# Kernel tuning notes

Measured on AMD Instinct MI355X. Metric: run time of the kernel, lower is better.

## Reference

```python
import jax, jax.numpy as jnp
import numpy as np
import math

S, B, D, H = 1024, 4, 1024, 16
DH = D // H


def setup_inputs() -> dict:
    key = jax.random.key(0)
    ks = jax.random.split(key, 8)
    hidden_states = jax.random.normal(ks[0], (S, B, D), dtype=jnp.float32)
    u = jax.random.uniform(ks[1], (B, 1, 1, S), dtype=jnp.float32)
    attention_mask = jnp.where(u < 0.2, jnp.float32(-10000.0), jnp.float32(0.0))
    std = 0.02
    Wq = jax.random.normal(ks[2], (D, D), dtype=jnp.float32) * std
    bq = jnp.zeros((D,), dtype=jnp.float32)
    Wk = jax.random.normal(ks[3], (D, D), dtype=jnp.float32) * std
    bk = jnp.zeros((D,), dtype=jnp.float32)
    Wv = jax.random.normal(ks[4], (D, D), dtype=jnp.float32) * std
    bv = jnp.zeros((D,), dtype=jnp.float32)
    return {"hidden_states": hidden_states, "attention_mask": attention_mask,
            "Wq": Wq, "bq": bq, "Wk": Wk, "bk": bk, "Wv": Wv, "bv": bv}


def _split_heads(x):
    # [S,B,D] -> [B,H,S,DH]
    s, b, d = x.shape
    return x.reshape(s, b, H, DH).transpose(1, 2, 0, 3)


def reference(hidden_states, attention_mask, Wq, bq, Wk, bk, Wv, bv):
    scale = 1.0 / math.sqrt(DH)
    q = _split_heads(hidden_states @ Wq.T + bq)  # [B,H,S,DH]
    k = _split_heads(hidden_states @ Wk.T + bk)
    v = _split_heads(hidden_states @ Wv.T + bv)
    # scaled scores + additive mask (mask [B,1,1,S] broadcasts over heads, query pos)
    scores = jnp.einsum('bhsd,bhtd->bhst', q, k) * scale + attention_mask  # [B,H,S,S]
    probs = jax.nn.softmax(scores, axis=-1)
    # NOTE: original forward's dropout block is a no-op (only reshapes), so none applied
    ctx = jnp.einsum('bhst,bhtd->bhsd', probs, v)  # [B,H,S,DH]
    # -> [S,B,D]
    return ctx.transpose(2, 0, 1, 3).reshape(S, B, D)
```

## Files before the change

### kernel.cpp

```cpp
#include <hip/hip_runtime.h>
#include <hip/hip_bf16.h>

#define S_LEN  1024
#define BATCH  4
#define DMODEL 1024
#define NHEAD  16
#define DHEAD  64
#define NROWS  (S_LEN*BATCH)

typedef __bf16 bf16;
typedef __bf16 bf16x4 __attribute__((ext_vector_type(4)));
typedef __bf16 bf16x8 __attribute__((ext_vector_type(8)));
typedef float  f32x4  __attribute__((ext_vector_type(4)));

#define AS1 __attribute__((address_space(1)))
#define AS3 __attribute__((address_space(3)))

__device__ __forceinline__ void gload16(const bf16* g, bf16* l) {
  __builtin_amdgcn_global_load_lds((const AS1 void*)g, (AS3 void*)l, 16, 0, 0);
}

__global__ __launch_bounds__(256) void cvt_all(
    const float* __restrict__ hs, const float* __restrict__ wq,
    const float* __restrict__ wk, const float* __restrict__ wv,
    bf16* __restrict__ Xb, bf16* __restrict__ Wb)
{
  const int b = blockIdx.x;
  const float* src; bf16* dst; int i;
  if (b < 2048)      { src = hs; dst = Xb;                           i = b*256        + threadIdx.x; }
  else if (b < 2560) { src = wq; dst = Wb;                           i = (b-2048)*256 + threadIdx.x; }
  else if (b < 3072) { src = wk; dst = Wb + (size_t)DMODEL*DMODEL;   i = (b-2560)*256 + threadIdx.x; }
  else               { src = wv; dst = Wb + (size_t)2*DMODEL*DMODEL; i = (b-3072)*256 + threadIdx.x; }
  const float4* s4 = (const float4*)src;
  float4 a = s4[2*i], c = s4[2*i+1];
  bf16x8 o;
  o[0]=(bf16)a.x; o[1]=(bf16)a.y; o[2]=(bf16)a.z; o[3]=(bf16)a.w;
  o[4]=(bf16)c.x; o[5]=(bf16)c.y; o[6]=(bf16)c.z; o[7]=(bf16)c.w;
  ((bf16x8*)dst)[i] = o;
}

#define BM 128
#define BN 128
#define BK 32

__global__ __launch_bounds__(256) void qkv_gemm(
    const bf16* __restrict__ X, const bf16* __restrict__ Wcat,
    const float* __restrict__ bq, const float* __restrict__ bk, const float* __restrict__ bv,
    bf16* __restrict__ Qo, bf16* __restrict__ Ko, bf16* __restrict__ Vo)
{
  __shared__ __align__(16) bf16 As[BM*BK];
  __shared__ __align__(16) bf16 Bs[BN*BK];

  const int tid  = threadIdx.x;
  const int row0 = blockIdx.x * BM;
  const int col0 = blockIdx.y * BN;
  const int wsel = col0 >> 10;
  const int coln = col0 & 1023;

  const int wv   = tid >> 6;
  const int lane = tid & 63;
  const int lg   = lane >> 4;
  const int lr   = lane & 15;
  const int wr   = (wv >> 1) << 6;
  const int wc   = (wv & 1) << 6;

  const int c0 = tid, c1 = tid + 256;
  const size_t gA0 = (size_t)(row0 + (c0>>2))*DMODEL + (size_t)((c0&3)<<3);
  const size_t gA1 = (size_t)(row0 + (c1>>2))*DMODEL + (size_t)((c1&3)<<3);
  const size_t gB0 = (size_t)(col0 + (c0>>2))*DMODEL + (size_t)((c0&3)<<3);
  const size_t gB1 = (size_t)(col0 + (c1>>2))*DMODEL + (size_t)((c1&3)<<3);
  const int wb = (tid >> 6) << 6;
  bf16* lA0 = As + (size_t)wb*8;
  bf16* lA1 = As + (size_t)(wb+256)*8;
  bf16* lB0 = Bs + (size_t)wb*8;
  bf16* lB1 = Bs + (size_t)(wb+256)*8;

  f32x4 acc[4][4];
  #pragma unroll
  for (int mi=0; mi<4; ++mi)
    #pragma unroll
    for (int ni=0; ni<4; ++ni)
      acc[mi][ni] = (f32x4){0.f,0.f,0.f,0.f};

  for (int k0 = 0; k0 < DMODEL; k0 += BK) {
    __syncthreads();
    gload16(X    + gA0 + k0, lA0);
    gload16(X    + gA1 + k0, lA1);
    gload16(Wcat + gB0 + k0, lB0);
    gload16(Wcat + gB1 + k0, lB1);
    __syncthreads();

    bf16x8 af[4], bfr[4];
    #pragma unroll
    for (int mi=0; mi<4; ++mi)
      af[mi] = *(const bf16x8*)&As[(wr + mi*16 + lr)*BK + lg*8];
    #pragma unroll
    for (int ni=0; ni<4; ++ni)
      bfr[ni] = *(const bf16x8*)&Bs[(wc + ni*16 + lr)*BK + lg*8];

    #pragma unroll
    for (int mi=0; mi<4; ++mi)
      #pragma unroll
      for (int ni=0; ni<4; ++ni)
        acc[mi][ni] = __builtin_amdgcn_mfma_f32_16x16x32_bf16(af[mi], bfr[ni], acc[mi][ni], 0, 0, 0);
  }

  const float* bias = (wsel==0) ? bq : ((wsel==1) ? bk : bv);
  bf16* Out = (wsel==0) ? Qo : ((wsel==1) ? Ko : Vo);

  #pragma unroll
  for (int ni=0; ni<4; ++ni) {
    const int co = coln + wc + ni*16 + lr;
    const float bias_v = bias[co];
    const int h  = co >> 6;
    const int dh = co & 63;
    #pragma unroll
    for (int mi=0; mi<4; ++mi) {
      #pragma unroll
      for (int p=0; p<4; ++p) {
        const int gr = row0 + wr + mi*16 + lg*4 + p;
        const int s_ = gr >> 2;
        const int b_ = gr & 3;
        Out[((size_t)(b_*NHEAD + h)*S_LEN + s_)*DHEAD + dh] = (bf16)(acc[mi][ni][p] + bias_v);
      }
    }
  }
}

#define LPAD 72

__global__ __launch_bounds__(256) void attn_mfma(
    const bf16* __restrict__ Q, const bf16* __restrict__ K, const bf16* __restrict__ V,
    const float* __restrict__ mask, float* __restrict__ out)
{
  __shared__ __align__(16) bf16 Qs[64][LPAD];
  __shared__ __align__(16) bf16 Ks[64][LPAD];
  __shared__ __align__(16) bf16 Vt[64][LPAD];
  __shared__ __align__(16) bf16 Pw[4][16][LPAD];
  __shared__ float Ms[64];

  const int bh   = blockIdx.x;
  const int b_   = bh >> 4;
  const int h    = bh & 15;
  const int tid  = threadIdx.x;
  const int wv   = tid >> 6;
  const int lane = tid & 63;
  const int lg   = lane >> 4;
  const int lr   = lane & 15;
  const int q0   = blockIdx.y * 64;

  const bf16* Qb = Q + ((size_t)bh*S_LEN + q0)*DHEAD;
  const bf16* Kb = K + (size_t)bh*S_LEN*DHEAD;
  const bf16* Vb = V + (size_t)bh*S_LEN*DHEAD;
  const float* mb = mask + (size_t)b_*S_LEN;

  {
    const int r = tid >> 2, c = (tid & 3) << 4;
    const bf16x8* src = (const bf16x8*)&Qb[(size_t)r*DHEAD + c];
    *(bf16x8*)&Qs[r][c]   = src[0];
    *(bf16x8*)&Qs[r][c+8] = src[1];
  }
  __syncthreads();
  bf16x8 qa0 = *(const bf16x8*)&Qs[wv*16 + lr][lg*8];
  bf16x8 qa1 = *(const bf16x8*)&Qs[wv*16 + lr][32 + lg*8];

  f32x4 ctx[4];
  #pragma unroll
  for (int nt=0; nt<4; ++nt) ctx[nt] = (f32x4){0.f,0.f,0.f,0.f};
  float lsum[4] = {0.f,0.f,0.f,0.f};

  const int vr = tid & 63, vc = (tid >> 6) << 4;

  for (int t0 = 0; t0 < S_LEN; t0 += 64) {
    __syncthreads();
    {
      const int r = tid >> 2, c = (tid & 3) << 4;
      const bf16x8* src = (const bf16x8*)&Kb[(size_t)(t0+r)*DHEAD + c];
      *(bf16x8*)&Ks[r][c]   = src[0];
      *(bf16x8*)&Ks[r][c+8] = src[1];
    }
    {
      const bf16x8* src = (const bf16x8*)&Vb[(size_t)(t0+vr)*DHEAD + vc];
      bf16x8 v0 = src[0], v1 = src[1];
      #pragma unroll
      for (int i=0;i<8;++i){ Vt[vc+i][vr] = v0[i]; Vt[vc+8+i][vr] = v1[i]; }
    }
    if (tid < 64) Ms[tid] = mb[t0 + tid];
    __syncthreads();

    f32x4 sacc[4];
    #pragma unroll
    for (int nt=0; nt<4; ++nt) {
      sacc[nt] = (f32x4){0.f,0.f,0.f,0.f};
      bf16x8 kb0 = *(const bf16x8*)&Ks[nt*16 + lr][lg*8];
      bf16x8 kb1 = *(const bf16x8*)&Ks[nt*16 + lr][32 + lg*8];
      sacc[nt] = __builtin_amdgcn_mfma_f32_16x16x32_bf16(qa0, kb0, sacc[nt], 0,0,0);
      sacc[nt] = __builtin_amdgcn_mfma_f32_16x16x32_bf16(qa1, kb1, sacc[nt], 0,0,0);
    }

    #pragma unroll
    for (int nt=0; nt<4; ++nt) {
      const float mval = Ms[nt*16 + lr];
      #pragma unroll
      for (int p=0; p<4; ++p) {
        const float pr = __expf(fmaf(sacc[nt][p], 0.125f, mval));
        lsum[p] += pr;
        Pw[wv][lg*4 + p][nt*16 + lr] = (bf16)pr;
      }
    }

    {
      bf16x8 pa0 = *(const bf16x8*)&Pw[wv][lr][lg*8];
      bf16x8 pa1 = *(const bf16x8*)&Pw[wv][lr][32 + lg*8];
      #pragma unroll
      for (int nt=0; nt<4; ++nt) {
        bf16x8 vb0 = *(const bf16x8*)&Vt[nt*16 + lr][lg*8];
        bf16x8 vb1 = *(const bf16x8*)&Vt[nt*16 + lr][32 + lg*8];
        ctx[nt] = __builtin_amdgcn_mfma_f32_16x16x32_bf16(pa0, vb0, ctx[nt], 0,0,0);
        ctx[nt] = __builtin_amdgcn_mfma_f32_16x16x32_bf16(pa1, vb1, ctx[nt], 0,0,0);
      }
    }
  }

  #pragma unroll
  for (int p=0; p<4; ++p) {
    float s = lsum[p];
    s += __shfl_xor(s, 1); s += __shfl_xor(s, 2);
    s += __shfl_xor(s, 4); s += __shfl_xor(s, 8);
    lsum[p] = s;
  }

  #pragma unroll
  for (int p=0; p<4; ++p) {
    const float inv = 1.f / lsum[p];
    const int qg = q0 + wv*16 + lg*4 + p;
    float* op = out + ((size_t)qg*BATCH + b_)*DMODEL + h*DHEAD;
    #pragma unroll
    for (int nt=0; nt<4; ++nt) op[nt*16 + lr] = ctx[nt][p] * inv;
  }
}

extern "C" void kernel_launch(void* const* d_in, const int* in_sizes, int n_in,
                              void* d_out, int out_size, void* d_ws, size_t ws_size,
                              hipStream_t stream) {
  const float* hs   = (const float*)d_in[0];
  const float* mask = (const float*)d_in[1];
  const float* Wq   = (const float*)d_in[2];
  const float* bq   = (const float*)d_in[3];
  const float* Wk   = (const float*)d_in[4];
  const float* bk   = (const float*)d_in[5];
  const float* Wv   = (const float*)d_in[6];
  const float* bv   = (const float*)d_in[7];
  float* out = (float*)d_out;

  char* ws = (char*)d_ws;
  bf16* Xb = (bf16*)ws;
  bf16* Wb = Xb + (size_t)NROWS*DMODEL;
  bf16* Qw = Wb + (size_t)3*DMODEL*DMODEL;
  bf16* Kw = Qw + (size_t)NROWS*DMODEL;
  bf16* Vw = Kw + (size_t)NROWS*DMODEL;

  cvt_all<<<3584, 256, 0, stream>>>(hs, Wq, Wk, Wv, Xb, Wb);

  qkv_gemm<<<dim3(NROWS/BM, 3*DMODEL/BN), 256, 0, stream>>>(Xb, Wb, bq, bk, bv, Qw, Kw, Vw);

  attn_mfma<<<dim3(BATCH*NHEAD, S_LEN/64), 256, 0, stream>>>(Qw, Kw, Vw, mask, out);
}
```

Measured before the change: 87.89 us.

## Prefetch K/V tiles into registers, fold softmax scale into Q, use exp2

The attention loop now prefetches the next K/V tile into registers while computing the current one, then writes it to shared memory after a barrier, so global load latency overlaps with compute. The softmax scale and log2(e) are folded into Q in the projection epilogue and into a bf16 copy of the whole mask row in shared memory, which allows a raw exp2 instead of fma plus exp. Q fragments are loaded straight from global memory into registers, and setprio hints and a launch-bounds occupancy target are added. In exchange, register pressure rises, and rounding the mask to bf16 and the pre-scaled Q to bf16 slightly changes precision.

```diff
diff --git a/kernel.cpp b/kernel.cpp
--- a/kernel.cpp
+++ b/kernel.cpp
@@ -16,8 +16,19 @@
 #define AS1 __attribute__((address_space(1)))
 #define AS3 __attribute__((address_space(3)))
 
+#define LOG2E   1.4426950408889634f
+#define QSCALE  0.18033688011112042f
+
 __device__ __forceinline__ void gload16(const bf16* g, bf16* l) {
   __builtin_amdgcn_global_load_lds((const AS1 void*)g, (AS3 void*)l, 16, 0, 0);
+}
+
+__device__ __forceinline__ float fast_exp2(float x) {
+#if __has_builtin(__builtin_amdgcn_exp2f)
+  return __builtin_amdgcn_exp2f(x);
+#else
+  return exp2f(x);
+#endif
 }
 
 __global__ __launch_bounds__(256) void cvt_all(
@@ -107,6 +118,7 @@
 
   const float* bias = (wsel==0) ? bq : ((wsel==1) ? bk : bv);
   bf16* Out = (wsel==0) ? Qo : ((wsel==1) ? Ko : Vo);
+  const float oscale = (wsel==0) ? QSCALE : 1.0f;
 
   #pragma unroll
   for (int ni=0; ni<4; ++ni) {
@@ -121,7 +133,7 @@
         const int gr = row0 + wr + mi*16 + lg*4 + p;
         const int s_ = gr >> 2;
         const int b_ = gr & 3;
-        Out[((size_t)(b_*NHEAD + h)*S_LEN + s_)*DHEAD + dh] = (bf16)(acc[mi][ni][p] + bias_v);
+        Out[((size_t)(b_*NHEAD + h)*S_LEN + s_)*DHEAD + dh] = (bf16)((acc[mi][ni][p] + bias_v) * oscale);
       }
     }
   }
@@ -129,15 +141,14 @@
 
 #define LPAD 72
 
-__global__ __launch_bounds__(256) void attn_mfma(
+__global__ __launch_bounds__(256, 4) void attn_mfma(
     const bf16* __restrict__ Q, const bf16* __restrict__ K, const bf16* __restrict__ V,
     const float* __restrict__ mask, float* __restrict__ out)
 {
-  __shared__ __align__(16) bf16 Qs[64][LPAD];
-  __shared__ __align__(16) bf16 Ks[64][LPAD];
-  __shared__ __align__(16) bf16 Vt[64][LPAD];
+  __shared__ __align__(16) bf16 Ks[64*LPAD];
+  __shared__ __align__(16) bf16 Vt[64*LPAD];
   __shared__ __align__(16) bf16 Pw[4][16][LPAD];
-  __shared__ float Ms[64];
+  __shared__ bf16 Msk[S_LEN];
 
   const int bh   = blockIdx.x;
   const int b_   = bh >> 4;
@@ -149,61 +160,67 @@
   const int lr   = lane & 15;
   const int q0   = blockIdx.y * 64;
 
-  const bf16* Qb = Q + ((size_t)bh*S_LEN + q0)*DHEAD;
+  {
+    const float4 m4 = *(const float4*)&mask[(size_t)b_*S_LEN + tid*4];
+    bf16x4 mm;
+    mm[0]=(bf16)(m4.x*LOG2E); mm[1]=(bf16)(m4.y*LOG2E);
+    mm[2]=(bf16)(m4.z*LOG2E); mm[3]=(bf16)(m4.w*LOG2E);
+    *(bf16x4*)&Msk[tid*4] = mm;
+  }
+
+  const bf16* Qb = Q + ((size_t)bh*S_LEN + q0 + wv*16 + lr)*DHEAD;
+  const bf16x8 qa0 = *(const bf16x8*)&Qb[lg*8];
+  const bf16x8 qa1 = *(const bf16x8*)&Qb[32 + lg*8];
+
   const bf16* Kb = K + (size_t)bh*S_LEN*DHEAD;
   const bf16* Vb = V + (size_t)bh*S_LEN*DHEAD;
-  const float* mb = mask + (size_t)b_*S_LEN;
-
-  {
-    const int r = tid >> 2, c = (tid & 3) << 4;
-    const bf16x8* src = (const bf16x8*)&Qb[(size_t)r*DHEAD + c];
-    *(bf16x8*)&Qs[r][c]   = src[0];
-    *(bf16x8*)&Qs[r][c+8] = src[1];
-  }
+
+  const int kr = tid >> 2, kc = (tid & 3) << 4;
+  const int vr = tid & 63, vc = (tid >> 6) << 4;
+
+  bf16x8 kreg0 = *(const bf16x8*)&Kb[(size_t)kr*DHEAD + kc];
+  bf16x8 kreg1 = *(const bf16x8*)&Kb[(size_t)kr*DHEAD + kc + 8];
+  bf16x8 vreg0 = *(const bf16x8*)&Vb[(size_t)vr*DHEAD + vc];
+  bf16x8 vreg1 = *(const bf16x8*)&Vb[(size_t)vr*DHEAD + vc + 8];
+  *(bf16x8*)&Ks[kr*LPAD + kc]     = kreg0;
+  *(bf16x8*)&Ks[kr*LPAD + kc + 8] = kreg1;
+  #pragma unroll
+  for (int i=0;i<8;++i){ Vt[(vc+i)*LPAD + vr] = vreg0[i]; Vt[(vc+8+i)*LPAD + vr] = vreg1[i]; }
   __syncthreads();
-  bf16x8 qa0 = *(const bf16x8*)&Qs[wv*16 + lr][lg*8];
-  bf16x8 qa1 = *(const bf16x8*)&Qs[wv*16 + lr][32 + lg*8];
 
   f32x4 ctx[4];
   #pragma unroll
   for (int nt=0; nt<4; ++nt) ctx[nt] = (f32x4){0.f,0.f,0.f,0.f};
   float lsum[4] = {0.f,0.f,0.f,0.f};
 
-  const int vr = tid & 63, vc = (tid >> 6) << 4;
-
-  for (int t0 = 0; t0 < S_LEN; t0 += 64) {
-    __syncthreads();
-    {
-      const int r = tid >> 2, c = (tid & 3) << 4;
-      const bf16x8* src = (const bf16x8*)&Kb[(size_t)(t0+r)*DHEAD + c];
-      *(bf16x8*)&Ks[r][c]   = src[0];
-      *(bf16x8*)&Ks[r][c+8] = src[1];
-    }
-    {
-      const bf16x8* src = (const bf16x8*)&Vb[(size_t)(t0+vr)*DHEAD + vc];
-      bf16x8 v0 = src[0], v1 = src[1];
-      #pragma unroll
-      for (int i=0;i<8;++i){ Vt[vc+i][vr] = v0[i]; Vt[vc+8+i][vr] = v1[i]; }
-    }
-    if (tid < 64) Ms[tid] = mb[t0 + tid];
-    __syncthreads();
+  for (int t = 0; t < 16; ++t) {
+    if (t < 15) {
+      const size_t nb = (size_t)(t+1)*64;
+      kreg0 = *(const bf16x8*)&Kb[(nb+kr)*DHEAD + kc];
+      kreg1 = *(const bf16x8*)&Kb[(nb+kr)*DHEAD + kc + 8];
+      vreg0 = *(const bf16x8*)&Vb[(nb+vr)*DHEAD + vc];
+      vreg1 = *(const bf16x8*)&Vb[(nb+vr)*DHEAD + vc + 8];
+    }
 
     f32x4 sacc[4];
+    __builtin_amdgcn_s_setprio(1);
     #pragma unroll
     for (int nt=0; nt<4; ++nt) {
       sacc[nt] = (f32x4){0.f,0.f,0.f,0.f};
-      bf16x8 kb0 = *(const bf16x8*)&Ks[nt*16 + lr][lg*8];
-      bf16x8 kb1 = *(const bf16x8*)&Ks[nt*16 + lr][32 + lg*8];
+      bf16x8 kb0 = *(const bf16x8*)&Ks[(nt*16 + lr)*LPAD + lg*8];
+      bf16x8 kb1 = *(const bf16x8*)&Ks[(nt*16 + lr)*LPAD + 32 + lg*8];
       sacc[nt] = __builtin_amdgcn_mfma_f32_16x16x32_bf16(qa0, kb0, sacc[nt], 0,0,0);
       sacc[nt] = __builtin_amdgcn_mfma_f32_16x16x32_bf16(qa1, kb1, sacc[nt], 0,0,0);
     }
-
+    __builtin_amdgcn_s_setprio(0);
+
+    const int tb = t*64;
     #pragma unroll
     for (int nt=0; nt<4; ++nt) {
-      const float mval = Ms[nt*16 + lr];
+      const float mval = (float)Msk[tb + nt*16 + lr];
       #pragma unroll
       for (int p=0; p<4; ++p) {
-        const float pr = __expf(fmaf(sacc[nt][p], 0.125f, mval));
+        const float pr = fast_exp2(sacc[nt][p] + mval);
         lsum[p] += pr;
         Pw[wv][lg*4 + p][nt*16 + lr] = (bf16)pr;
       }
@@ -212,13 +229,24 @@
     {
       bf16x8 pa0 = *(const bf16x8*)&Pw[wv][lr][lg*8];
       bf16x8 pa1 = *(const bf16x8*)&Pw[wv][lr][32 + lg*8];
+      __builtin_amdgcn_s_setprio(1);
       #pragma unroll
       for (int nt=0; nt<4; ++nt) {
-        bf16x8 vb0 = *(const bf16x8*)&Vt[nt*16 + lr][lg*8];
-        bf16x8 vb1 = *(const bf16x8*)&Vt[nt*16 + lr][32 + lg*8];
+        bf16x8 vb0 = *(const bf16x8*)&Vt[(nt*16 + lr)*LPAD + lg*8];
+        bf16x8 vb1 = *(const bf16x8*)&Vt[(nt*16 + lr)*LPAD + 32 + lg*8];
         ctx[nt] = __builtin_amdgcn_mfma_f32_16x16x32_bf16(pa0, vb0, ctx[nt], 0,0,0);
         ctx[nt] = __builtin_amdgcn_mfma_f32_16x16x32_bf16(pa1, vb1, ctx[nt], 0,0,0);
       }
+      __builtin_amdgcn_s_setprio(0);
+    }
+
+    __syncthreads();
+    if (t < 15) {
+      *(bf16x8*)&Ks[kr*LPAD + kc]     = kreg0;
+      *(bf16x8*)&Ks[kr*LPAD + kc + 8] = kreg1;
+      #pragma unroll
+      for (int i=0;i<8;++i){ Vt[(vc+i)*LPAD + vr] = vreg0[i]; Vt[(vc+8+i)*LPAD + vr] = vreg1[i]; }
+      __syncthreads();
     }
   }
 
```

New measurement: 83.37 us. 5.1% less time.
